# Kernel tuning notes

Hardware: AMD Instinct MI355X
Metric: run time of the kernel (lower is better)

The kernel has to match this reference:

```python
import jax, jax.numpy as jnp
import numpy as np

B, N, K, D, F, H = 8, 512, 16, 256, 1024, 8


def _ln(x, g, b):
    m = jnp.mean(x, axis=-1, keepdims=True)
    v = jnp.var(x, axis=-1, keepdims=True)
    return (x - m) / jnp.sqrt(v + 1e-5) * g + b


def _mlp(x, W1, b1, W2, b2):
    return jax.nn.gelu(x @ W1 + b1, approximate=False) @ W2 + b2


def setup_inputs() -> dict:
    key = jax.random.key(0)
    ks = jax.random.split(key, 16)
    s = 0.02
    inp = {
        'x': jax.random.normal(ks[0], (N, B, D), jnp.float32),
        'e': jax.random.normal(ks[1], (B, N, K, D), jnp.float32),
        'edge_index': jax.random.randint(ks[2], (B, N, K), 0, N),
        'Wq': jax.random.normal(ks[3], (D, D), jnp.float32) * s,
        'bq': jnp.zeros((D,), jnp.float32),
        'Wk': jax.random.normal(ks[4], (D, D), jnp.float32) * s,
        'bk': jnp.zeros((D,), jnp.float32),
        'Wv': jax.random.normal(ks[5], (D, D), jnp.float32) * s,
        'bv': jnp.zeros((D,), jnp.float32),
        'Wo': jax.random.normal(ks[6], (D, D), jnp.float32) * s,
        'bo': jnp.zeros((D,), jnp.float32),
        'nW1': jax.random.normal(ks[7], (D, F), jnp.float32) * s,
        'nb1': jnp.zeros((F,), jnp.float32),
        'nW2': jax.random.normal(ks[8], (F, D), jnp.float32) * s,
        'nb2': jnp.zeros((D,), jnp.float32),
        'eW1': jax.random.normal(ks[9], (D, F), jnp.float32) * s,
        'eb1': jnp.zeros((F,), jnp.float32),
        'eW2': jax.random.normal(ks[10], (F, D), jnp.float32) * s,
        'eb2': jnp.zeros((D,), jnp.float32),
        'na_g': jnp.ones((D,), jnp.float32), 'na_b': jnp.zeros((D,), jnp.float32),
        'ea_g': jnp.ones((D,), jnp.float32), 'ea_b': jnp.zeros((D,), jnp.float32),
        'nf_g': jnp.ones((D,), jnp.float32), 'nf_b': jnp.zeros((D,), jnp.float32),
        'ef_g': jnp.ones((D,), jnp.float32), 'ef_b': jnp.zeros((D,), jnp.float32),
    }
    return inp


def reference(x, e, edge_index, Wq, bq, Wk, bk, Wv, bv, Wo, bo,
              nW1, nb1, nW2, nb2, eW1, eb1, eW2, eb2,
              na_g, na_b, ea_g, ea_b, nf_g, nf_b, ef_g, ef_b):
    n, b, d = x.shape
    hd = d // H
    xt = jnp.transpose(x, (1, 0, 2))  # (B, N, D) residual in batch-first layout
    bi = jnp.arange(b)[:, None, None]
    ni = jnp.arange(n)[None, :, None]

    # scatter edge features into dense additive attention bias (B, N, N)
    attn_bias = jnp.zeros((b, n, n), x.dtype).at[bi, ni, edge_index].set(e.mean(-1))

    def heads(t):  # (B,N,D) -> (B,H,N,hd)
        return t.reshape(b, n, H, hd).transpose(0, 2, 1, 3)

    q = heads(xt @ Wq + bq) * (hd ** -0.5)
    k = heads(xt @ Wk + bk)
    v = heads(xt @ Wv + bv)
    logits = jnp.einsum('bhnd,bhmd->bhnm', q, k) + attn_bias[:, None]
    attn = jax.nn.softmax(logits, axis=-1)  # (B,H,N,N)
    out = jnp.einsum('bhnm,bhmd->bhnd', attn, v)
    out = out.transpose(0, 2, 1, 3).reshape(b, n, d) @ Wo + bo

    xn = _ln(xt + out, na_g, na_b)  # (B,N,D)

    # edge update: gather attn weights and neighbor node features via edge_index
    weights = attn.mean(axis=1)  # (B,N,N) head-averaged
    w = weights[bi, edge_index, ni]  # (B,N,K): weights[b, edge_index[b,n,k], n]
    gathered = xt[jnp.arange(b)[:, None, None], edge_index]  # (B,N,K,D)
    e2 = _ln(e + w[..., None] * gathered, ea_g, ea_b)

    xn = _ln(xn + _mlp(xn, nW1, nb1, nW2, nb2), nf_g, nf_b)
    e2 = _ln(e2 + _mlp(e2, eW1, eb1, eW2, eb2), ef_g, ef_b)
    return jnp.transpose(xn, (1, 0, 2)), e2
```

## Files before the change

kernel.cpp:

```cpp
#include <hip/hip_runtime.h>
#include <hip/hip_bf16.h>
#include <math.h>

#define B_ 8
#define N_ 512
#define K_ 16
#define D_ 256
#define F_ 1024
#define H_ 8
#define HD_ 32
#define M_ (B_*N_)
#define R_ (B_*N_*K_)

typedef __bf16 bf16x8 __attribute__((ext_vector_type(8)));
typedef float  f32x4  __attribute__((ext_vector_type(4)));

__device__ inline short bf16s(float f) {
    __hip_bfloat16 h = __float2bfloat16(f);
    return *reinterpret_cast<short*>(&h);
}
__device__ inline float b2f(short s) {
    union { float f; unsigned u; } v; v.u = ((unsigned)(unsigned short)s) << 16; return v.f;
}

__device__ __forceinline__ void gload16(const short* g, short* l) {
    __builtin_amdgcn_global_load_lds(
        (const __attribute__((address_space(1))) unsigned int*)g,
        (__attribute__((address_space(3))) unsigned int*)l, 16, 0, 0);
}

__global__ __launch_bounds__(256) void transposeAll(
        const float* __restrict__ Wq, const float* __restrict__ Wk,
        const float* __restrict__ Wv, const float* __restrict__ Wo,
        const float* __restrict__ nW1, const float* __restrict__ nW2,
        const float* __restrict__ eW1, const float* __restrict__ eW2,
        short* __restrict__ WqkvT, short* __restrict__ WoT,
        short* __restrict__ nW1T, short* __restrict__ nW2T,
        short* __restrict__ eW1T, short* __restrict__ eW2T)
{
    const float* W; short* WT; int Kk, Nn; float sc = 1.f;
    switch (blockIdx.z) {
        case 0: W=Wq;  WT=WqkvT;          Kk=256;  Nn=256;  sc=0.17677669529663687f; break;
        case 1: W=Wk;  WT=WqkvT+256*256;  Kk=256;  Nn=256;  break;
        case 2: W=Wv;  WT=WqkvT+512*256;  Kk=256;  Nn=256;  break;
        case 3: W=Wo;  WT=WoT;            Kk=256;  Nn=256;  break;
        case 4: W=nW1; WT=nW1T;           Kk=256;  Nn=1024; break;
        case 5: W=nW2; WT=nW2T;           Kk=1024; Nn=256;  break;
        case 6: W=eW1; WT=eW1T;           Kk=256;  Nn=1024; break;
        default:W=eW2; WT=eW2T;           Kk=1024; Nn=256;  break;
    }
    const int bx = blockIdx.x, by = blockIdx.y;
    if (bx >= Nn/32 || by >= Kk/32) return;
    __shared__ float tile[32][33];
    int tx = threadIdx.x & 31, ty = threadIdx.x >> 5;
    #pragma unroll
    for (int j = 0; j < 4; ++j) {
        int k = by*32 + ty + j*8;
        tile[ty + j*8][tx] = W[(size_t)k*Nn + bx*32 + tx];
    }
    __syncthreads();
    #pragma unroll
    for (int j = 0; j < 4; ++j) {
        int n = bx*32 + ty + j*8;
        WT[(size_t)n*Kk + by*32 + tx] = bf16s(tile[tx][ty + j*8] * sc);
    }
}

__global__ __launch_bounds__(256) void build_bqkv(const float* __restrict__ bq,
        const float* __restrict__ bk, const float* __restrict__ bv,
        float* __restrict__ bqkv)
{
    int t = blockIdx.x*256 + threadIdx.x;
    if (t >= 768) return;
    float v = (t < 256) ? bq[t]*0.17677669529663687f
            : (t < 512) ? bk[t-256] : bv[t-512];
    bqkv[t] = v;
}

__global__ __launch_bounds__(256) void conv_x(const float* __restrict__ x,
        short* __restrict__ xtb)
{
    int row = blockIdx.x;
    int d = threadIdx.x;
    int b = row >> 9, n = row & 511;
    xtb[(size_t)row*D_ + d] = bf16s(x[((size_t)n*B_ + b)*D_ + d]);
}

__global__ __launch_bounds__(256) void edge_means(const float* __restrict__ e,
        float* __restrict__ means)
{
    long row = (long)blockIdx.x*4 + (threadIdx.x >> 6);
    int lane = threadIdx.x & 63;
    float4 v = ((const float4*)(e + row*D_))[lane];
    float s = v.x + v.y + v.z + v.w;
    for (int o = 1; o < 64; o <<= 1) s += __shfl_xor(s, o);
    if (lane == 0) means[row] = s * (1.f/D_);
}

__global__ __launch_bounds__(256) void bias_build(const int* __restrict__ ei,
        const float* __restrict__ means, float* __restrict__ biasb)
{
    const int r0 = blockIdx.x * 16;
    float4* bp4 = (float4*)(biasb + (size_t)r0*N_);
    #pragma unroll
    for (int i = threadIdx.x; i < 16*N_/4; i += 256)
        bp4[i] = make_float4(0.f, 0.f, 0.f, 0.f);
    __syncthreads();
    if (threadIdx.x < 16) {
        const int idx = r0 + threadIdx.x;
        const int* ep = ei + (size_t)idx*K_;
        const float* mp = means + (size_t)idx*K_;
        float* bp = biasb + (size_t)idx*N_;
        for (int k = 0; k < K_; ++k) bp[ep[k]] = mp[k];
    }
}

__global__ __launch_bounds__(256) void gemm_qkv(
        const short* __restrict__ A, const short* __restrict__ BT,
        const float* __restrict__ bias, short* __restrict__ Cb,
        short* __restrict__ vtb, int Kk)
{
    __shared__ __align__(16) short As[128*32];
    __shared__ __align__(16) short Bs[128*32];
    const int t = threadIdx.x;
    const int lane = t & 63;
    const int wave = t >> 6;
    const int wr = (wave >> 1) * 64;
    const int wc = (wave & 1) * 64;
    const int bm = blockIdx.x, bn = blockIdx.y;
    f32x4 acc[4][4] = {};
    const int srow = lane >> 2;
    const int sk   = (lane & 3) * 8;
    const int fr = lane & 15;
    const int fk = (lane >> 4) * 8;
    for (int k0 = 0; k0 < Kk; k0 += 32) {
        __syncthreads();
        #pragma unroll
        for (int i = 0; i < 2; ++i) {
            const int rb = wave*16 + i*64;
            gload16(A  + (size_t)(bm*128 + rb + srow)*Kk + k0 + sk, &As[rb*32]);
            gload16(BT + (size_t)(bn*128 + rb + srow)*Kk + k0 + sk, &Bs[rb*32]);
        }
        __syncthreads();
        bf16x8 af[4], bfr[4];
        #pragma unroll
        for (int i2 = 0; i2 < 4; ++i2)
            af[i2] = *(const bf16x8*)&As[(wr + i2*16 + fr)*32 + fk];
        #pragma unroll
        for (int n2 = 0; n2 < 4; ++n2)
            bfr[n2] = *(const bf16x8*)&Bs[(wc + n2*16 + fr)*32 + fk];
        #pragma unroll
        for (int i2 = 0; i2 < 4; ++i2)
            #pragma unroll
            for (int n2 = 0; n2 < 4; ++n2)
                acc[i2][n2] = __builtin_amdgcn_mfma_f32_16x16x32_bf16(
                        af[i2], bfr[n2], acc[i2][n2], 0, 0, 0);
    }
    const int fq4 = (lane >> 4) * 4;
    #pragma unroll
    for (int i2 = 0; i2 < 4; ++i2) {
        #pragma unroll
        for (int n2 = 0; n2 < 4; ++n2) {
            const int col = bn*128 + wc + n2*16 + fr;
            const float bv = bias[col];
            const int rowb = bm*128 + wr + i2*16 + fq4;
            if (col < 512) {
                #pragma unroll
                for (int r2 = 0; r2 < 4; ++r2)
                    Cb[(size_t)(rowb + r2)*512 + col] = bf16s(acc[i2][n2][r2] + bv);
            } else {
                const int b = rowb >> 9, n = rowb & 511;
                const int dv = col - 512, h = dv >> 5, dh = dv & 31;
                short4 s4;
                s4.x = bf16s(acc[i2][n2][0] + bv);
                s4.y = bf16s(acc[i2][n2][1] + bv);
                s4.z = bf16s(acc[i2][n2][2] + bv);
                s4.w = bf16s(acc[i2][n2][3] + bv);
                *(short4*)&vtb[((size_t)((b*H_ + h)*HD_ + dh))*512 + n] = s4;
            }
        }
    }
}

__global__ __launch_bounds__(512, 4) void gemm_gelu(
        const short* __restrict__ A, const short* __restrict__ BT,
        const float* __restrict__ bias, short* __restrict__ Cb, int Nn, int Kk)
{
    __shared__ __align__(16) short As[2][128*32];
    __shared__ __align__(16) short Bs[2][256*32];
    const int t = threadIdx.x;
    const int lane = t & 63;
    const int wave = t >> 6;
    const int wrg = (wave >> 2) * 64;
    const int wc  = (wave & 3) * 64;
    const int bm = blockIdx.x, bn = blockIdx.y;
    f32x4 acc[4][4] = {};
    const int srow = lane >> 2;
    const int sk   = (lane & 3) * 8;
    const int fr = lane & 15;
    const int fk = (lane >> 4) * 8;
    auto stage = [&](int s, int k0) {
        {
            const int rb = wave*16;
            gload16(A + (size_t)(bm*128 + rb + srow)*Kk + k0 + sk, &As[s][rb*32]);
        }
        #pragma unroll
        for (int i = 0; i < 2; ++i) {
            const int rb = wave*16 + i*128;
            gload16(BT + (size_t)(bn*256 + rb + srow)*Kk + k0 + sk, &Bs[s][rb*32]);
        }
    };
    stage(0, 0);
    __syncthreads();
    int cur = 0;
    for (int k0 = 0; k0 < Kk; k0 += 32) {
        if (k0 + 32 < Kk) stage(cur ^ 1, k0 + 32);
        bf16x8 af[4], bfr[4];
        #pragma unroll
        for (int i2 = 0; i2 < 4; ++i2)
            af[i2] = *(const bf16x8*)&As[cur][(wrg + i2*16 + fr)*32 + fk];
        #pragma unroll
        for (int n2 = 0; n2 < 4; ++n2)
            bfr[n2] = *(const bf16x8*)&Bs[cur][(wc + n2*16 + fr)*32 + fk];
        #pragma unroll
        for (int i2 = 0; i2 < 4; ++i2)
            #pragma unroll
            for (int n2 = 0; n2 < 4; ++n2)
                acc[i2][n2] = __builtin_amdgcn_mfma_f32_16x16x32_bf16(
                        af[i2], bfr[n2], acc[i2][n2], 0, 0, 0);
        __syncthreads();
        cur ^= 1;
    }
    const int fq4 = (lane >> 4) * 4;
    #pragma unroll
    for (int i2 = 0; i2 < 4; ++i2) {
        #pragma unroll
        for (int n2 = 0; n2 < 4; ++n2) {
            const int col = bn*256 + wc + n2*16 + fr;
            const float bv = bias[col];
            #pragma unroll
            for (int r2 = 0; r2 < 4; ++r2) {
                const int row = bm*128 + wrg + i2*16 + fq4 + r2;
                float v = acc[i2][n2][r2] + bv;
                v = 0.5f*v*(1.f + erff(v*0.70710678118654752f));
                Cb[(size_t)row*Nn + col] = bf16s(v);
            }
        }
    }
}

template<bool TRANSOUT, int RESMODE, bool DUALOUT>
__global__ __launch_bounds__(512, 4) void gemm_ln2(
        const short* __restrict__ A, const short* __restrict__ BT,
        const float* __restrict__ bias, const float* __restrict__ resf,
        const short* __restrict__ resb,
        const float* __restrict__ g, const float* __restrict__ bt,
        float* __restrict__ out, short* __restrict__ outb, int Kk)
{
    __shared__ __align__(16) short As[2][128*32];
    __shared__ __align__(16) short Bs[2][256*32];
    __shared__ float rs[128][4][2];
    __shared__ float mr[128][2];
    const int t = threadIdx.x;
    const int lane = t & 63;
    const int wave = t >> 6;
    const int wrg = (wave >> 2) * 64;
    const int wc  = (wave & 3) * 64;
    const int bm = blockIdx.x;
    f32x4 acc[4][4] = {};
    const int srow = lane >> 2;
    const int sk   = (lane & 3) * 8;
    const int fr = lane & 15;
    const int fk = (lane >> 4) * 8;
    auto stage = [&](int s, int k0) {
        {
            const int rb = wave*16;
            gload16(A + (size_t)(bm*128 + rb + srow)*Kk + k0 + sk, &As[s][rb*32]);
        }
        #pragma unroll
        for (int i = 0; i < 2; ++i) {
            const int rb = wave*16 + i*128;
            gload16(BT + (size_t)(rb + srow)*Kk + k0 + sk, &Bs[s][rb*32]);
        }
    };
    stage(0, 0);
    __syncthreads();
    int cur = 0;
    for (int k0 = 0; k0 < Kk; k0 += 32) {
        if (k0 + 32 < Kk) stage(cur ^ 1, k0 + 32);
        bf16x8 af[4], bfr[4];
        #pragma unroll
        for (int i2 = 0; i2 < 4; ++i2)
            af[i2] = *(const bf16x8*)&As[cur][(wrg + i2*16 + fr)*32 + fk];
        #pragma unroll
        for (int n2 = 0; n2 < 4; ++n2)
            bfr[n2] = *(const bf16x8*)&Bs[cur][(wc + n2*16 + fr)*32 + fk];
        #pragma unroll
        for (int i2 = 0; i2 < 4; ++i2)
            #pragma unroll
            for (int n2 = 0; n2 < 4; ++n2)
                acc[i2][n2] = __builtin_amdgcn_mfma_f32_16x16x32_bf16(
                        af[i2], bfr[n2], acc[i2][n2], 0, 0, 0);
        __syncthreads();
        cur ^= 1;
    }
    const int fq4 = (lane >> 4) * 4;
    float ps[4][4] = {}, pq[4][4] = {};
    #pragma unroll
    for (int i2 = 0; i2 < 4; ++i2) {
        #pragma unroll
        for (int n2 = 0; n2 < 4; ++n2) {
            const int c = wc + n2*16 + fr;
            const float bv = bias[c];
            #pragma unroll
            for (int r2 = 0; r2 < 4; ++r2) {
                const int row = wrg + i2*16 + fq4 + r2;
                const size_t grow = (size_t)bm*128 + row;
                float rv;
                if constexpr (RESMODE == 1) rv = b2f(resb[grow*256 + c]);
                else if constexpr (RESMODE == 2) {
                    const int bb = (int)(grow >> 9), nn = (int)(grow & 511);
                    rv = resf[((size_t)nn*B_ + bb)*256 + c];
                } else rv = resf[grow*256 + c];
                float v = acc[i2][n2][r2] + bv + rv;
                acc[i2][n2][r2] = v;
                ps[i2][r2] += v;
                pq[i2][r2] += v*v;
            }
        }
    }
    #pragma unroll
    for (int i2 = 0; i2 < 4; ++i2)
        #pragma unroll
        for (int r2 = 0; r2 < 4; ++r2)
            #pragma unroll
            for (int o = 1; o < 16; o <<= 1) {
                ps[i2][r2] += __shfl_xor(ps[i2][r2], o);
                pq[i2][r2] += __shfl_xor(pq[i2][r2], o);
            }
    if ((lane & 15) == 0) {
        #pragma unroll
        for (int i2 = 0; i2 < 4; ++i2)
            #pragma unroll
            for (int r2 = 0; r2 < 4; ++r2) {
                const int row = wrg + i2*16 + fq4 + r2;
                rs[row][wave & 3][0] = ps[i2][r2];
                rs[row][wave & 3][1] = pq[i2][r2];
            }
    }
    __syncthreads();
    if (t < 128) {
        float S = 0.f, Q = 0.f;
        #pragma unroll
        for (int w = 0; w < 4; ++w) { S += rs[t][w][0]; Q += rs[t][w][1]; }
        const float mean = S * (1.f/D_);
        mr[t][0] = mean;
        mr[t][1] = rsqrtf(Q * (1.f/D_) - mean*mean + 1e-5f);
    }
    __syncthreads();
    #pragma unroll
    for (int i2 = 0; i2 < 4; ++i2) {
        #pragma unroll
        for (int n2 = 0; n2 < 4; ++n2) {
            const int c = wc + n2*16 + fr;
            const float gv = g[c], bv2 = bt[c];
            #pragma unroll
            for (int r2 = 0; r2 < 4; ++r2) {
                const int row = wrg + i2*16 + fq4 + r2;
                const size_t grow = (size_t)bm*128 + row;
                const float o = (acc[i2][n2][r2] - mr[row][0])*mr[row][1]*gv + bv2;
                if constexpr (TRANSOUT) {
                    const int bb = (int)(grow >> 9), nn = (int)(grow & 511);
                    out[((size_t)nn*B_ + bb)*D_ + c] = o;
                } else {
                    out[grow*256 + c] = o;
                }
                if constexpr (DUALOUT)
                    outb[grow*256 + c] = bf16s(o);
            }
        }
    }
}

__global__ __launch_bounds__(256) void attn_fused(const short* __restrict__ qkb,
        const short* __restrict__ vtb, const float* __restrict__ biasb,
        float* __restrict__ rowsum, short* __restrict__ actx)
{
    __shared__ __align__(16) short Qs[128*32];
    __shared__ __align__(16) short Ks[128*32];
    __shared__ __align__(16) short Vs[32*128];
    __shared__ __align__(16) short Ps[128*128];
    const int it = blockIdx.x, bh = blockIdx.y;
    const int b = bh >> 3, h = bh & 7;
    const int t = threadIdx.x;
    const int lane = t & 63;
    const int wave = t >> 6;
    const int wr0 = wave * 32;
    const int srow = lane >> 2;
    const int sk   = (lane & 3) * 8;
    const int srow8 = lane >> 4;
    const int ck16  = lane & 15;
    const int fr = lane & 15;
    const int fk = (lane >> 4) * 8;
    const int fq4 = (lane >> 4) * 4;
    const int I0 = it * 128;
    #pragma unroll
    for (int i = 0; i < 2; ++i) {
        const int rb = wave*16 + i*64;
        gload16(qkb + (size_t)(b*N_ + I0 + rb + srow)*512 + h*HD_ + sk, &Qs[rb*32]);
    }
    float rsum[2][4] = {};
    f32x4 apv[2][2] = {};
    const float LOG2E = 1.4426950408889634f;
    for (int jt = 0; jt < 4; ++jt) {
        const int J0 = jt * 128;
        __syncthreads();
        #pragma unroll
        for (int i = 0; i < 2; ++i) {
            const int rb = wave*16 + i*64;
            gload16(qkb + (size_t)(b*N_ + J0 + rb + srow)*512 + 256 + h*HD_ + sk, &Ks[rb*32]);
        }
        #pragma unroll
        for (int i = 0; i < 2; ++i) {
            const int db = wave*8 + i*4;
            const int dh = db + srow8;
            gload16(vtb + ((size_t)bh*HD_ + dh)*512 + J0 + ((ck16 ^ (dh & 7)) * 8),
                    &Vs[db*128]);
        }
        __syncthreads();
        bf16x8 aq[2], kf8[8];
        #pragma unroll
        for (int i2 = 0; i2 < 2; ++i2)
            aq[i2] = *(const bf16x8*)&Qs[(wr0 + i2*16 + fr)*32 + fk];
        #pragma unroll
        for (int n2 = 0; n2 < 8; ++n2)
            kf8[n2] = *(const bf16x8*)&Ks[(n2*16 + fr)*32 + fk];
        #pragma unroll
        for (int i2 = 0; i2 < 2; ++i2) {
            #pragma unroll
            for (int n2 = 0; n2 < 8; ++n2) {
                f32x4 z = {0.f, 0.f, 0.f, 0.f};
                f32x4 s = __builtin_amdgcn_mfma_f32_16x16x32_bf16(aq[i2], kf8[n2], z, 0, 0, 0);
                const int jg = J0 + n2*16 + fr;
                #pragma unroll
                for (int r2 = 0; r2 < 4; ++r2) {
                    const int rloc = wr0 + i2*16 + fq4 + r2;
                    const float l = s[r2] + biasb[((size_t)b*N_ + I0 + rloc)*N_ + jg];
                    const float p = exp2f(fminf(l, 80.f) * LOG2E);
                    rsum[i2][r2] += p;
                    int idx = rloc*128 + n2*16 + fr;
                    idx ^= (rloc & 7) << 3;
                    Ps[idx] = bf16s(p);
                }
            }
        }
        __syncthreads();
        #pragma unroll
        for (int ks = 0; ks < 4; ++ks) {
            bf16x8 ap[2], bv[2];
            #pragma unroll
            for (int i2 = 0; i2 < 2; ++i2) {
                const int r = wr0 + i2*16 + fr;
                int idx = r*128 + ks*32 + fk;
                idx ^= (r & 7) << 3;
                ap[i2] = *(const bf16x8*)&Ps[idx];
            }
            #pragma unroll
            for (int n2 = 0; n2 < 2; ++n2) {
                const int dh = n2*16 + fr;
                const int q = lane >> 4;
                const int slot = (ks*4 + q) ^ (dh & 7);
                bv[n2] = *(const bf16x8*)&Vs[dh*128 + slot*8];
            }
            #pragma unroll
            for (int i2 = 0; i2 < 2; ++i2)
                #pragma unroll
                for (int n2 = 0; n2 < 2; ++n2)
                    apv[i2][n2] = __builtin_amdgcn_mfma_f32_16x16x32_bf16(
                            ap[i2], bv[n2], apv[i2][n2], 0, 0, 0);
        }
    }
    #pragma unroll
    for (int i2 = 0; i2 < 2; ++i2)
        #pragma unroll
        for (int r2 = 0; r2 < 4; ++r2)
            #pragma unroll
            for (int o = 1; o < 16; o <<= 1)
                rsum[i2][r2] += __shfl_xor(rsum[i2][r2], o);
    #pragma unroll
    for (int i2 = 0; i2 < 2; ++i2) {
        #pragma unroll
        for (int r2 = 0; r2 < 4; ++r2) {
            const int row = wr0 + i2*16 + fq4 + r2;
            if (fr == 0)
                rowsum[(size_t)bh*N_ + I0 + row] = rsum[i2][r2];
            const float inv = 1.f / rsum[i2][r2];
            #pragma unroll
            for (int n2 = 0; n2 < 2; ++n2)
                actx[((size_t)b*N_ + I0 + row)*D_ + h*HD_ + n2*16 + fr]
                    = bf16s(apv[i2][n2][r2] * inv);
        }
    }
}

__device__ inline void ln_core(float v[4], int lane, const float* __restrict__ g,
        const float* __restrict__ bt, float out[4])
{
    float s  = v[0] + v[1] + v[2] + v[3];
    float sq = v[0]*v[0] + v[1]*v[1] + v[2]*v[2] + v[3]*v[3];
    for (int o = 1; o < 64; o <<= 1) { s += __shfl_xor(s, o); sq += __shfl_xor(sq, o); }
    float mean = s * (1.f/D_);
    float rstd = rsqrtf(sq * (1.f/D_) - mean*mean + 1e-5f);
    const float4 gv = *(const float4*)(g  + lane*4);
    const float4 bv = *(const float4*)(bt + lane*4);
    out[0] = (v[0]-mean)*rstd*gv.x + bv.x;
    out[1] = (v[1]-mean)*rstd*gv.y + bv.y;
    out[2] = (v[2]-mean)*rstd*gv.z + bv.z;
    out[3] = (v[3]-mean)*rstd*gv.w + bv.w;
}

__global__ __launch_bounds__(256) void edge_update(const float* __restrict__ e,
        const float* __restrict__ x, const int* __restrict__ ei,
        const short* __restrict__ qkb, const float* __restrict__ biasb,
        const float* __restrict__ rowsum, const float* __restrict__ g,
        const float* __restrict__ bt, short* __restrict__ e2b)
{
    long row = (long)blockIdx.x*4 + (threadIdx.x >> 6);
    int lane = threadIdx.x & 63;
    long bi = row >> 4;
    long b = bi / N_; int i = (int)(bi % N_);
    int ej = ei[row];
    const short4 q4 = *(const short4*)(qkb + ((size_t)b*N_ + ej)*512 + lane*4);
    const short4 k4 = *(const short4*)(qkb + ((size_t)b*N_ + i)*512 + 256 + lane*4);
    float dot = b2f(q4.x)*b2f(k4.x) + b2f(q4.y)*b2f(k4.y)
              + b2f(q4.z)*b2f(k4.z) + b2f(q4.w)*b2f(k4.w);
    dot += __shfl_xor(dot, 1); dot += __shfl_xor(dot, 2); dot += __shfl_xor(dot, 4);
    const int h = lane >> 3;
    const float l = dot + biasb[((size_t)b*N_ + ej)*N_ + i];
    float p = exp2f(fminf(l, 80.f) * 1.4426950408889634f)
            / rowsum[((size_t)b*H_ + h)*N_ + ej];
    p += __shfl_xor(p, 8); p += __shfl_xor(p, 16); p += __shfl_xor(p, 32);
    const float w = p * (1.f/H_);
    const float4 ev = *(const float4*)(e + row*D_ + lane*4);
    const float4 xv = *(const float4*)(x + ((size_t)ej*B_ + b)*D_ + lane*4);
    float v[4] = {ev.x + w*xv.x, ev.y + w*xv.y, ev.z + w*xv.z, ev.w + w*xv.w};
    float o[4];
    ln_core(v, lane, g, bt, o);
    short4 s4; s4.x = bf16s(o[0]); s4.y = bf16s(o[1]); s4.z = bf16s(o[2]); s4.w = bf16s(o[3]);
    *(short4*)(e2b + row*D_ + lane*4) = s4;
}

extern "C" void kernel_launch(void* const* d_in, const int* in_sizes, int n_in,
                              void* d_out, int out_size, void* d_ws, size_t ws_size,
                              hipStream_t stream)
{
    (void)in_sizes; (void)n_in; (void)out_size; (void)ws_size;
    const float* x    = (const float*)d_in[0];
    const float* e    = (const float*)d_in[1];
    const int*   ei   = (const int*)d_in[2];
    const float* Wq   = (const float*)d_in[3];
    const float* bq   = (const float*)d_in[4];
    const float* Wk   = (const float*)d_in[5];
    const float* bk   = (const float*)d_in[6];
    const float* Wv   = (const float*)d_in[7];
    const float* bv   = (const float*)d_in[8];
    const float* Wo   = (const float*)d_in[9];
    const float* bo   = (const float*)d_in[10];
    const float* nW1  = (const float*)d_in[11];
    const float* nb1  = (const float*)d_in[12];
    const float* nW2  = (const float*)d_in[13];
    const float* nb2  = (const float*)d_in[14];
    const float* eW1  = (const float*)d_in[15];
    const float* eb1  = (const float*)d_in[16];
    const float* eW2  = (const float*)d_in[17];
    const float* eb2  = (const float*)d_in[18];
    const float* na_g = (const float*)d_in[19];
    const float* na_b = (const float*)d_in[20];
    const float* ea_g = (const float*)d_in[21];
    const float* ea_b = (const float*)d_in[22];
    const float* nf_g = (const float*)d_in[23];
    const float* nf_b = (const float*)d_in[24];
    const float* ef_g = (const float*)d_in[25];
    const float* ef_b = (const float*)d_in[26];

    float* out1 = (float*)d_out;
    float* e2f  = out1 + (size_t)N_*B_*D_;

    char* wp = (char*)d_ws;
    auto alloc = [&](size_t bytes) -> char* {
        char* p = wp; wp += (bytes + 255) & ~(size_t)255; return p;
    };
    short* WqkvT  = (short*)alloc((size_t)768*D_*2);
    float* bqkv   = (float*)alloc(768*4);
    short* WoT    = (short*)alloc((size_t)D_*D_*2);
    short* nW1T   = (short*)alloc((size_t)F_*D_*2);
    short* nW2T   = (short*)alloc((size_t)D_*F_*2);
    short* eW1T   = (short*)alloc((size_t)F_*D_*2);
    short* eW2T   = (short*)alloc((size_t)D_*F_*2);
    float* rowsum = (float*)alloc((size_t)B_*H_*N_*4);
    short* e2b    = (short*)alloc((size_t)R_*D_*2);
    char* ov = wp;
    auto allocA = [&](size_t bytes) -> char* {
        char* p = ov; ov += (bytes + 255) & ~(size_t)255; return p;
    };
    short* xtb    = (short*)allocA((size_t)M_*D_*2);
    float* means  = (float*)allocA((size_t)R_*4);
    float* biasb  = (float*)allocA((size_t)B_*N_*N_*4);
    short* qkb    = (short*)allocA((size_t)M_*512*2);
    short* vtb    = (short*)allocA((size_t)B_*H_*HD_*N_*2);
    short* actx   = (short*)allocA((size_t)M_*D_*2);
    float* xn     = (float*)allocA((size_t)M_*D_*4);
    short* xnb    = (short*)allocA((size_t)M_*D_*2);
    short* nhid   = (short*)allocA((size_t)M_*F_*2);
    short* ehid   = (short*)wp;

    transposeAll<<<dim3(32, 32, 8), 256, 0, stream>>>(Wq, Wk, Wv, Wo,
            nW1, nW2, eW1, eW2, WqkvT, WoT, nW1T, nW2T, eW1T, eW2T);
    build_bqkv<<<3, 256, 0, stream>>>(bq, bk, bv, bqkv);
    conv_x<<<M_, 256, 0, stream>>>(x, xtb);

    edge_means<<<R_/4, 256, 0, stream>>>(e, means);
    bias_build<<<M_/16, 256, 0, stream>>>(ei, means, biasb);

    gemm_qkv<<<dim3(M_/128, 768/128), 256, 0, stream>>>(
            xtb, WqkvT, bqkv, qkb, vtb, D_);

    attn_fused<<<dim3(N_/128, B_*H_), 256, 0, stream>>>(qkb, vtb, biasb, rowsum, actx);

    gemm_ln2<false,2,true><<<M_/128, 512, 0, stream>>>(
            actx, WoT, bo, x, nullptr, na_g, na_b, xn, xnb, D_);

    gemm_gelu<<<dim3(M_/128, F_/256), 512, 0, stream>>>(
            xnb, nW1T, nb1, nhid, F_, D_);
    gemm_ln2<true,0,false><<<M_/128, 512, 0, stream>>>(
            nhid, nW2T, nb2, xn, nullptr, nf_g, nf_b, out1, nullptr, F_);

    edge_update<<<R_/4, 256, 0, stream>>>(e, x, ei, qkb, biasb, rowsum,
            ea_g, ea_b, e2b);
    gemm_gelu<<<dim3(R_/128, F_/256), 512, 0, stream>>>(
            e2b, eW1T, eb1, ehid, F_, D_);
    gemm_ln2<false,1,false><<<R_/128, 512, 0, stream>>>(
            ehid, eW2T, eb2, nullptr, e2b, ef_g, ef_b, e2f, nullptr, F_);
}
```

Before: 328.9 us.

## Quantize edge MLP hidden activations and second weight to FP8 for down-projection

The edge MLP's GELU output is now stored as FP8 e4m3 (scaled by 16) and eW2 is transposed into FP8 (scaled by 64). A new GEMM+LayerNorm kernel uses fp8 MFMA with 64-wide K tiles and rescales by 1/1024. This halves the traffic of the largest intermediate (R×F hidden) and doubles the MFMA rate for the biggest GEMM. The cost is reduced precision, with a risk of accuracy tolerance failures or overflow and underflow from the fixed scales.

```diff
diff --git a/kernel.cpp b/kernel.cpp
--- a/kernel.cpp
+++ b/kernel.cpp
@@ -1,5 +1,6 @@
 #include <hip/hip_runtime.h>
 #include <hip/hip_bf16.h>
+#include <hip/hip_fp8.h>
 #include <math.h>
 
 #define B_ 8
@@ -22,8 +23,13 @@
 __device__ inline float b2f(short s) {
     union { float f; unsigned u; } v; v.u = ((unsigned)(unsigned short)s) << 16; return v.f;
 }
-
-__device__ __forceinline__ void gload16(const short* g, short* l) {
+__device__ inline unsigned char f8e4m3(float f) {
+    union { __hip_fp8_e4m3 h; unsigned char c; } u;
+    u.h = __hip_fp8_e4m3(f);
+    return u.c;
+}
+
+__device__ __forceinline__ void gload16(const void* g, void* l) {
     __builtin_amdgcn_global_load_lds(
         (const __attribute__((address_space(1))) unsigned int*)g,
         (__attribute__((address_space(3))) unsigned int*)l, 16, 0, 0);
@@ -36,9 +42,9 @@
         const float* __restrict__ eW1, const float* __restrict__ eW2,
         short* __restrict__ WqkvT, short* __restrict__ WoT,
         short* __restrict__ nW1T, short* __restrict__ nW2T,
-        short* __restrict__ eW1T, short* __restrict__ eW2T)
-{
-    const float* W; short* WT; int Kk, Nn; float sc = 1.f;
+        short* __restrict__ eW1T, unsigned char* __restrict__ eW2T8)
+{
+    const float* W; short* WT = nullptr; int Kk, Nn; float sc = 1.f;
     switch (blockIdx.z) {
         case 0: W=Wq;  WT=WqkvT;          Kk=256;  Nn=256;  sc=0.17677669529663687f; break;
         case 1: W=Wk;  WT=WqkvT+256*256;  Kk=256;  Nn=256;  break;
@@ -47,7 +53,7 @@
         case 4: W=nW1; WT=nW1T;           Kk=256;  Nn=1024; break;
         case 5: W=nW2; WT=nW2T;           Kk=1024; Nn=256;  break;
         case 6: W=eW1; WT=eW1T;           Kk=256;  Nn=1024; break;
-        default:W=eW2; WT=eW2T;           Kk=1024; Nn=256;  break;
+        default:W=eW2;                    Kk=1024; Nn=256;  break;
     }
     const int bx = blockIdx.x, by = blockIdx.y;
     if (bx >= Nn/32 || by >= Kk/32) return;
@@ -59,10 +65,18 @@
         tile[ty + j*8][tx] = W[(size_t)k*Nn + bx*32 + tx];
     }
     __syncthreads();
-    #pragma unroll
-    for (int j = 0; j < 4; ++j) {
-        int n = bx*32 + ty + j*8;
-        WT[(size_t)n*Kk + by*32 + tx] = bf16s(tile[tx][ty + j*8] * sc);
+    if (blockIdx.z == 7) {
+        #pragma unroll
+        for (int j = 0; j < 4; ++j) {
+            int n = bx*32 + ty + j*8;
+            eW2T8[(size_t)n*Kk + by*32 + tx] = f8e4m3(tile[tx][ty + j*8] * 64.f);
+        }
+    } else {
+        #pragma unroll
+        for (int j = 0; j < 4; ++j) {
+            int n = bx*32 + ty + j*8;
+            WT[(size_t)n*Kk + by*32 + tx] = bf16s(tile[tx][ty + j*8] * sc);
+        }
     }
 }
 
@@ -182,9 +196,11 @@
     }
 }
 
+template<bool F8>
 __global__ __launch_bounds__(512, 4) void gemm_gelu(
         const short* __restrict__ A, const short* __restrict__ BT,
-        const float* __restrict__ bias, short* __restrict__ Cb, int Nn, int Kk)
+        const float* __restrict__ bias, short* __restrict__ Cb,
+        unsigned char* __restrict__ C8, int Nn, int Kk)
 {
     __shared__ __align__(16) short As[2][128*32];
     __shared__ __align__(16) short Bs[2][256*32];
@@ -243,7 +259,8 @@
                 const int row = bm*128 + wrg + i2*16 + fq4 + r2;
                 float v = acc[i2][n2][r2] + bv;
                 v = 0.5f*v*(1.f + erff(v*0.70710678118654752f));
-                Cb[(size_t)row*Nn + col] = bf16s(v);
+                if constexpr (F8) C8[(size_t)row*Nn + col] = f8e4m3(v * 16.f);
+                else              Cb[(size_t)row*Nn + col] = bf16s(v);
             }
         }
     }
@@ -377,6 +394,128 @@
                 }
                 if constexpr (DUALOUT)
                     outb[grow*256 + c] = bf16s(o);
+            }
+        }
+    }
+}
+
+__global__ __launch_bounds__(512, 4) void gemm_ln2f8(
+        const unsigned char* __restrict__ A, const unsigned char* __restrict__ BT,
+        const float* __restrict__ bias, const short* __restrict__ resb,
+        const float* __restrict__ g, const float* __restrict__ bt,
+        float* __restrict__ out)
+{
+    __shared__ __align__(16) unsigned char As[2][128*64];
+    __shared__ __align__(16) unsigned char Bs[2][256*64];
+    __shared__ float rs[128][4][2];
+    __shared__ float mr[128][2];
+    const int t = threadIdx.x;
+    const int lane = t & 63;
+    const int wave = t >> 6;
+    const int wrg = (wave >> 2) * 64;
+    const int wc  = (wave & 3) * 64;
+    const int bm = blockIdx.x;
+    f32x4 acc[4][4] = {};
+    const int srow = lane >> 2;
+    const int skb  = (lane & 3) * 16;
+    const int fr  = lane & 15;
+    const int fk8 = (lane >> 4) * 8;
+    auto stage = [&](int s, int k0) {
+        {
+            const int rb = wave*16;
+            gload16(A + (size_t)(bm*128 + rb + srow)*1024 + k0 + skb, &As[s][rb*64]);
+        }
+        #pragma unroll
+        for (int i = 0; i < 2; ++i) {
+            const int rb = wave*16 + i*128;
+            gload16(BT + (size_t)(rb + srow)*1024 + k0 + skb, &Bs[s][rb*64]);
+        }
+    };
+    stage(0, 0);
+    __syncthreads();
+    int cur = 0;
+    for (int k0 = 0; k0 < 1024; k0 += 64) {
+        if (k0 + 64 < 1024) stage(cur ^ 1, k0 + 64);
+        long a8[2][4], b8[2][4];
+        #pragma unroll
+        for (int s = 0; s < 2; ++s) {
+            #pragma unroll
+            for (int i2 = 0; i2 < 4; ++i2)
+                a8[s][i2] = *(const long*)&As[cur][(wrg + i2*16 + fr)*64 + s*32 + fk8];
+            #pragma unroll
+            for (int n2 = 0; n2 < 4; ++n2)
+                b8[s][n2] = *(const long*)&Bs[cur][(wc + n2*16 + fr)*64 + s*32 + fk8];
+        }
+        #pragma unroll
+        for (int s = 0; s < 2; ++s)
+            #pragma unroll
+            for (int i2 = 0; i2 < 4; ++i2)
+                #pragma unroll
+                for (int n2 = 0; n2 < 4; ++n2)
+                    acc[i2][n2] = __builtin_amdgcn_mfma_f32_16x16x32_fp8_fp8(
+                            a8[s][i2], b8[s][n2], acc[i2][n2], 0, 0, 0);
+        __syncthreads();
+        cur ^= 1;
+    }
+    const int fq4 = (lane >> 4) * 4;
+    float ps[4][4] = {}, pq[4][4] = {};
+    #pragma unroll
+    for (int i2 = 0; i2 < 4; ++i2) {
+        #pragma unroll
+        for (int n2 = 0; n2 < 4; ++n2) {
+            const int c = wc + n2*16 + fr;
+            const float bv = bias[c];
+            #pragma unroll
+            for (int r2 = 0; r2 < 4; ++r2) {
+                const int row = wrg + i2*16 + fq4 + r2;
+                const size_t grow = (size_t)bm*128 + row;
+                float v = acc[i2][n2][r2]*(1.f/1024.f) + bv + b2f(resb[grow*256 + c]);
+                acc[i2][n2][r2] = v;
+                ps[i2][r2] += v;
+                pq[i2][r2] += v*v;
+            }
+        }
+    }
+    #pragma unroll
+    for (int i2 = 0; i2 < 4; ++i2)
+        #pragma unroll
+        for (int r2 = 0; r2 < 4; ++r2)
+            #pragma unroll
+            for (int o = 1; o < 16; o <<= 1) {
+                ps[i2][r2] += __shfl_xor(ps[i2][r2], o);
+                pq[i2][r2] += __shfl_xor(pq[i2][r2], o);
+            }
+    if ((lane & 15) == 0) {
+        #pragma unroll
+        for (int i2 = 0; i2 < 4; ++i2)
+            #pragma unroll
+            for (int r2 = 0; r2 < 4; ++r2) {
+                const int row = wrg + i2*16 + fq4 + r2;
+                rs[row][wave & 3][0] = ps[i2][r2];
+                rs[row][wave & 3][1] = pq[i2][r2];
+            }
+    }
+    __syncthreads();
+    if (t < 128) {
+        float S = 0.f, Q = 0.f;
+        #pragma unroll
+        for (int w = 0; w < 4; ++w) { S += rs[t][w][0]; Q += rs[t][w][1]; }
+        const float mean = S * (1.f/D_);
+        mr[t][0] = mean;
+        mr[t][1] = rsqrtf(Q * (1.f/D_) - mean*mean + 1e-5f);
+    }
+    __syncthreads();
+    #pragma unroll
+    for (int i2 = 0; i2 < 4; ++i2) {
+        #pragma unroll
+        for (int n2 = 0; n2 < 4; ++n2) {
+            const int c = wc + n2*16 + fr;
+            const float gv = g[c], bv2 = bt[c];
+            #pragma unroll
+            for (int r2 = 0; r2 < 4; ++r2) {
+                const int row = wrg + i2*16 + fq4 + r2;
+                const size_t grow = (size_t)bm*128 + row;
+                out[grow*256 + c] = (acc[i2][n2][r2] - mr[row][0])*mr[row][1]*gv + bv2;
             }
         }
     }
@@ -596,7 +735,7 @@
     short* nW1T   = (short*)alloc((size_t)F_*D_*2);
     short* nW2T   = (short*)alloc((size_t)D_*F_*2);
     short* eW1T   = (short*)alloc((size_t)F_*D_*2);
-    short* eW2T   = (short*)alloc((size_t)D_*F_*2);
+    unsigned char* eW2T8 = (unsigned char*)alloc((size_t)D_*F_);
     float* rowsum = (float*)alloc((size_t)B_*H_*N_*4);
     short* e2b    = (short*)alloc((size_t)R_*D_*2);
     char* ov = wp;
@@ -612,10 +751,10 @@
     float* xn     = (float*)allocA((size_t)M_*D_*4);
     short* xnb    = (short*)allocA((size_t)M_*D_*2);
     short* nhid   = (short*)allocA((size_t)M_*F_*2);
-    short* ehid   = (short*)wp;
+    unsigned char* ehid8 = (unsigned char*)wp;
 
     transposeAll<<<dim3(32, 32, 8), 256, 0, stream>>>(Wq, Wk, Wv, Wo,
-            nW1, nW2, eW1, eW2, WqkvT, WoT, nW1T, nW2T, eW1T, eW2T);
+            nW1, nW2, eW1, eW2, WqkvT, WoT, nW1T, nW2T, eW1T, eW2T8);
     build_bqkv<<<3, 256, 0, stream>>>(bq, bk, bv, bqkv);
     conv_x<<<M_, 256, 0, stream>>>(x, xtb);
 
@@ -630,15 +769,15 @@
     gemm_ln2<false,2,true><<<M_/128, 512, 0, stream>>>(
             actx, WoT, bo, x, nullptr, na_g, na_b, xn, xnb, D_);
 
-    gemm_gelu<<<dim3(M_/128, F_/256), 512, 0, stream>>>(
-            xnb, nW1T, nb1, nhid, F_, D_);
+    gemm_gelu<false><<<dim3(M_/128, F_/256), 512, 0, stream>>>(
+            xnb, nW1T, nb1, nhid, nullptr, F_, D_);
     gemm_ln2<true,0,false><<<M_/128, 512, 0, stream>>>(
             nhid, nW2T, nb2, xn, nullptr, nf_g, nf_b, out1, nullptr, F_);
 
     edge_update<<<R_/4, 256, 0, stream>>>(e, x, ei, qkb, biasb, rowsum,
             ea_g, ea_b, e2b);
-    gemm_gelu<<<dim3(R_/128, F_/256), 512, 0, stream>>>(
-            e2b, eW1T, eb1, ehid, F_, D_);
-    gemm_ln2<false,1,false><<<R_/128, 512, 0, stream>>>(
-            ehid, eW2T, eb2, nullptr, e2b, ef_g, ef_b, e2f, nullptr, F_);
-}
+    gemm_gelu<true><<<dim3(R_/128, F_/256), 512, 0, stream>>>(
+            e2b, eW1T, eb1, nullptr, ehid8, F_, D_);
+    gemm_ln2f8<<<R_/128, 512, 0, stream>>>(
+            ehid8, eW2T8, eb2, e2b, ef_g, ef_b, e2f);
+}
```

Result: slower. 356.6 us (+8.4%).
